# Kernel optimization log

Measured on AMD Instinct MI355X. Metric: run time of the kernel, lower is better.

The kernel has to match this reference:

```python
import math
import jax, jax.numpy as jnp
import numpy as np

N = 8192
IN_DIM = 512
INTER = 512
HID = 1024
OUT = 512
GROUPS = 16
EPS = 1e-5


def setup_inputs() -> dict:
    key = jax.random.key(0)
    ks = jax.random.split(key, 12)
    w = lambda k, shape: jax.random.normal(k, shape, jnp.float32) * 0.02
    return {
        "h": jax.random.normal(ks[0], (N, IN_DIM), jnp.float32),
        "D": jax.random.uniform(ks[1], (N, N), dtype=jnp.float32),
        "h_prime": jax.random.normal(ks[2], (N, OUT), jnp.float32),
        "Wq": w(ks[3], (INTER, IN_DIM)), "bq": jnp.zeros((INTER,), jnp.float32),
        "Wk": w(ks[4], (INTER, IN_DIM)), "bk": jnp.zeros((INTER,), jnp.float32),
        "Wv": w(ks[5], (INTER, IN_DIM)), "bv": jnp.zeros((INTER,), jnp.float32),
        "Wr": w(ks[6], (HID, INTER)), "br": jnp.zeros((HID,), jnp.float32),
        "Wc": w(ks[7], (HID, OUT)), "bc": jnp.zeros((HID,), jnp.float32),
        "Wp": w(ks[8], (OUT, 2 * HID)), "bp": jnp.zeros((OUT,), jnp.float32),
        "alpha": jnp.full((OUT,), 0.25, jnp.float32),       # PReLU per-channel slope
        "gamma": jnp.ones((OUT,), jnp.float32),             # GroupNorm weight
        "beta": jnp.zeros((OUT,), jnp.float32),             # GroupNorm bias
    }


def reference(h, D, h_prime, Wq, bq, Wk, bk, Wv, bv, Wr, br, Wc, bc, Wp, bp, alpha, gamma, beta):
    Q = h @ Wq.T + bq                                    # [N, inter]
    K = h @ Wk.T + bk
    V = h @ Wv.T + bv
    scores = (Q @ K.T) / math.sqrt(INTER)                # [N, N]
    attn = jax.nn.softmax(D * scores, axis=-1)           # decay-masked softmax
    h_ret = attn @ V                                     # [N, inter]
    h_ret = jax.nn.gelu(h_ret @ Wr.T + br, approximate=False)  # torch GELU (erf)
    h_cat = h_prime @ Wc.T + bc                          # [N, hid]
    x = jnp.concatenate([h_ret, h_cat], axis=-1) @ Wp.T + bp   # [N, out]
    x = jnp.where(x >= 0, x, alpha * x)                  # PReLU, per-channel
    # GroupNorm over [1, out, N]: stats per group over (channels_in_group, N)
    xT = x.T                                             # [out, N]
    grp = xT.reshape(GROUPS, (OUT // GROUPS) * N)
    mean = grp.mean(axis=1, keepdims=True)
    var = grp.var(axis=1, keepdims=True)
    grp = (grp - mean) * jax.lax.rsqrt(var + EPS)
    xT = grp.reshape(OUT, N) * gamma[:, None] + beta[:, None]
    return xT.T                                          # [N, out]
```

## Files before the change

kernel.cpp:

```cpp
#include <hip/hip_runtime.h>
#include <stdint.h>
#include <math.h>

typedef float f32x4 __attribute__((ext_vector_type(4)));
typedef __bf16 bf16x8 __attribute__((ext_vector_type(8)));
typedef unsigned int u32x4 __attribute__((ext_vector_type(4)));
typedef unsigned short u16;

#define DEVINL static __device__ __forceinline__

DEVINL u16 f2bf(float f) {
  union { float f; unsigned u; } x; x.f = f;
  unsigned r = x.u + 0x7fffu + ((x.u >> 16) & 1u);
  return (u16)(r >> 16);
}

DEVINL void gload_lds16(const void* g, void* l) {
  __builtin_amdgcn_global_load_lds(
      (__attribute__((address_space(1))) void*)(g),
      (__attribute__((address_space(3))) void*)(l), 16, 0, 0);
}

__global__ void cast_kernel(const float* __restrict__ src, u16* __restrict__ dst, int n) {
  int i = (blockIdx.x * 256 + threadIdx.x) * 4;
  if (i >= n) return;
  float4 v = *(const float4*)(src + i);
  u16 o[4] = { f2bf(v.x), f2bf(v.y), f2bf(v.z), f2bf(v.w) };
  *(uint64_t*)(dst + i) = *(uint64_t*)o;
}

template<int EPI>
__global__ __launch_bounds__(256, 2) void gemm_nt(
    const u16* __restrict__ A, int lda, const u16* __restrict__ B, int ldb,
    void* __restrict__ C, int ldc, int coff,
    const float* __restrict__ bias, const float* __restrict__ alpha,
    int N128, int K, float scale, int map,
    const float* __restrict__ Dmat, float* __restrict__ psum)
{
  __shared__ __align__(16) u16 at[2][128 * 64];
  __shared__ __align__(16) u16 bt[2][128 * 64];
  const int tid = threadIdx.x;
  const int w = tid >> 6, lane = tid & 63, r = lane & 15, kg = lane >> 4;
  int bm, bn;
  if (map == 1)      { const int x = blockIdx.x & 7, i = blockIdx.x >> 3; bm = x * 8 + (i >> 2); bn = i & 3; }
  else if (map == 2) { const int x = blockIdx.x & 7, i = blockIdx.x >> 3; bm = x * 8 + (i >> 6); bn = i & 63; }
  else               { bm = blockIdx.x / N128; bn = blockIdx.x % N128; }
  const int m0 = bm * 128, n0 = bn * 128;

  f32x4 acc[4][4];
  #pragma unroll
  for (int m = 0; m < 4; ++m)
    #pragma unroll
    for (int n = 0; n < 4; ++n) acc[m][n] = f32x4{0.f, 0.f, 0.f, 0.f};

  const int srow = tid >> 3, sc = tid & 7;
  const int nk = K >> 6;

  #pragma unroll
  for (int i = 0; i < 4; ++i) {
    int row = srow + i * 32, cs = (sc ^ row) & 7;
    gload_lds16(A + (size_t)(m0 + row) * lda + cs * 8, at[0] + i * 2048 + w * 512);
    gload_lds16(B + (size_t)(n0 + row) * ldb + cs * 8, bt[0] + i * 2048 + w * 512);
  }
  __syncthreads();

  for (int kt = 0; kt < nk; ++kt) {
    const int cur = kt & 1;
    if (kt + 1 < nk) {
      #pragma unroll
      for (int i = 0; i < 4; ++i) {
        int row = srow + i * 32, cs = (sc ^ row) & 7;
        int kcol = (kt + 1) * 64 + cs * 8;
        gload_lds16(A + (size_t)(m0 + row) * lda + kcol, at[cur ^ 1] + i * 2048 + w * 512);
        gload_lds16(B + (size_t)(n0 + row) * ldb + kcol, bt[cur ^ 1] + i * 2048 + w * 512);
      }
    }
    #pragma unroll
    for (int ks = 0; ks < 2; ++ks) {
      bf16x8 af[4], bff[4];
      #pragma unroll
      for (int m = 0; m < 4; ++m) {
        int row = (w >> 1) * 64 + m * 16 + r;
        int cs = ((ks * 4 + kg) ^ row) & 7;
        af[m] = *(const bf16x8*)(at[cur] + row * 64 + cs * 8);
      }
      #pragma unroll
      for (int n = 0; n < 4; ++n) {
        int row = (w & 1) * 64 + n * 16 + r;
        int cs = ((ks * 4 + kg) ^ row) & 7;
        bff[n] = *(const bf16x8*)(bt[cur] + row * 64 + cs * 8);
      }
      #pragma unroll
      for (int m = 0; m < 4; ++m)
        #pragma unroll
        for (int n = 0; n < 4; ++n)
          acc[m][n] = __builtin_amdgcn_mfma_f32_16x16x32_bf16(af[m], bff[n], acc[m][n], 0, 0, 0);
    }
    __syncthreads();
  }

  if (EPI == 6) {
    #pragma unroll
    for (int m = 0; m < 4; ++m) {
      float rs[4] = {0.f, 0.f, 0.f, 0.f};
      #pragma unroll
      for (int n = 0; n < 4; ++n) {
        const int gcol = n0 + (w & 1) * 64 + n * 16 + r;
        #pragma unroll
        for (int reg = 0; reg < 4; ++reg) {
          const int grow = m0 + (w >> 1) * 64 + m * 16 + kg * 4 + reg;
          const float dv = __builtin_nontemporal_load(Dmat + (size_t)grow * 8192 + gcol);
          const float p = __expf(acc[m][n][reg] * dv);
          rs[reg] += p;
          ((u16*)C)[(size_t)grow * ldc + gcol] = f2bf(p);
        }
      }
      #pragma unroll
      for (int reg = 0; reg < 4; ++reg) {
        float v = rs[reg];
        v += __shfl_xor(v, 1); v += __shfl_xor(v, 2);
        v += __shfl_xor(v, 4); v += __shfl_xor(v, 8);
        if (r == 0) {
          const int grow = m0 + (w >> 1) * 64 + m * 16 + kg * 4 + reg;
          psum[(size_t)grow * 128 + bn * 2 + (w & 1)] = v;
        }
      }
    }
    return;
  }

  #pragma unroll
  for (int m = 0; m < 4; ++m) {
    #pragma unroll
    for (int n = 0; n < 4; ++n) {
      const int gcol = n0 + (w & 1) * 64 + n * 16 + r;
      #pragma unroll
      for (int reg = 0; reg < 4; ++reg) {
        const int grow = m0 + (w >> 1) * 64 + m * 16 + kg * 4 + reg;
        float v = acc[m][n][reg];
        if (EPI == 0) v = (v + bias[gcol]) * scale;
        if (EPI == 1) v = v + bias[grow];
        if (EPI == 2) { v += bias[gcol]; v = 0.5f * v * (1.f + erff(v * 0.70710678118654752f)); }
        if (EPI == 5) v = v / bias[grow];
        if (EPI == 3) {
          v += bias[gcol];
          float a = alpha[gcol];
          v = (v >= 0.f) ? v : a * v;
          ((float*)C)[(size_t)grow * ldc + coff + gcol] = v;
        } else {
          ((u16*)C)[(size_t)grow * ldc + coff + gcol] = f2bf(v);
        }
      }
    }
  }
}

__global__ __launch_bounds__(256) void rowsum_kernel(const float* __restrict__ psum,
                                                     float* __restrict__ ls) {
  const int row = blockIdx.x * 4 + (threadIdx.x >> 6);
  const int lane = threadIdx.x & 63;
  const float2 v = *(const float2*)(psum + (size_t)row * 128 + lane * 2);
  float s = v.x + v.y;
  #pragma unroll
  for (int m = 1; m < 64; m <<= 1) s += __shfl_xor(s, m);
  if (lane == 0) ls[row] = s;
}

__global__ void gn_stats_kernel(const float* __restrict__ x, float* __restrict__ part) {
  const int g = blockIdx.x >> 4, ch = blockIdx.x & 15;
  const int t = threadIdx.x;
  float s = 0.f, ss = 0.f;
  const int cl = (t & 7) * 4;
  const int r0 = ch * 512 + (t >> 3);
  for (int i = 0; i < 16; ++i) {
    const float4 v = *(const float4*)(x + (size_t)(r0 + i * 32) * 512 + g * 32 + cl);
    s += v.x + v.y + v.z + v.w;
    ss += v.x * v.x + v.y * v.y + v.z * v.z + v.w * v.w;
  }
  #pragma unroll
  for (int m = 1; m < 64; m <<= 1) { s += __shfl_xor(s, m); ss += __shfl_xor(ss, m); }
  __shared__ float red[8];
  const int w = t >> 6, lane = t & 63;
  if (lane == 0) { red[w * 2] = s; red[w * 2 + 1] = ss; }
  __syncthreads();
  if (t == 0) {
    part[blockIdx.x * 2]     = red[0] + red[2] + red[4] + red[6];
    part[blockIdx.x * 2 + 1] = red[1] + red[3] + red[5] + red[7];
  }
}

__global__ void gn_finalize_kernel(const float* __restrict__ part, float* __restrict__ mv) {
  const int g = threadIdx.x;
  if (g < 16) {
    float s = 0.f, ss = 0.f;
    for (int ch = 0; ch < 16; ++ch) {
      s  += part[(g * 16 + ch) * 2];
      ss += part[(g * 16 + ch) * 2 + 1];
    }
    const float mean = s * (1.f / 262144.f);
    const float var = ss * (1.f / 262144.f) - mean * mean;
    mv[g * 2] = mean;
    mv[g * 2 + 1] = rsqrtf(var + 1e-5f);
  }
}

__global__ void gn_norm_kernel(const float* __restrict__ x, const float* __restrict__ mv,
                               const float* __restrict__ gamma, const float* __restrict__ beta,
                               float* __restrict__ out) {
  const int idx = (blockIdx.x * 256 + threadIdx.x) * 4;
  const int c = idx & 511, g = c >> 5;
  const float mean = mv[g * 2], rs = mv[g * 2 + 1];
  float4 v = *(const float4*)(x + idx);
  const float4 gm = *(const float4*)(gamma + c);
  const float4 bt = *(const float4*)(beta + c);
  v.x = (v.x - mean) * rs * gm.x + bt.x;
  v.y = (v.y - mean) * rs * gm.y + bt.y;
  v.z = (v.z - mean) * rs * gm.z + bt.z;
  v.w = (v.w - mean) * rs * gm.w + bt.w;
  *(float4*)(out + idx) = v;
}

extern "C" void kernel_launch(void* const* d_in, const int* in_sizes, int n_in,
                              void* d_out, int out_size, void* d_ws, size_t ws_size,
                              hipStream_t stream) {
  (void)in_sizes; (void)n_in; (void)out_size; (void)ws_size;
  const float* h     = (const float*)d_in[0];
  const float* Dm    = (const float*)d_in[1];
  const float* hp    = (const float*)d_in[2];
  const float* Wq    = (const float*)d_in[3];
  const float* bq    = (const float*)d_in[4];
  const float* Wk    = (const float*)d_in[5];
  const float* bk    = (const float*)d_in[6];
  const float* Wv    = (const float*)d_in[7];
  const float* bv    = (const float*)d_in[8];
  const float* Wr    = (const float*)d_in[9];
  const float* br    = (const float*)d_in[10];
  const float* Wc    = (const float*)d_in[11];
  const float* bc    = (const float*)d_in[12];
  const float* Wp    = (const float*)d_in[13];
  const float* bp    = (const float*)d_in[14];
  const float* alpha = (const float*)d_in[15];
  const float* gamma = (const float*)d_in[16];
  const float* beta  = (const float*)d_in[17];

  char* ws = (char*)d_ws;
  const size_t MB = 1ull << 20;
  u16*   P    = (u16*)(ws);
  u16*   hb   = (u16*)(ws);
  u16*   xcat = (u16*)(ws);
  float* xf   = (float*)(ws + 32 * MB);
  u16*   hpb  = (u16*)(ws + 128 * MB);
  u16*   Qb   = (u16*)(ws + 144 * MB);
  u16*   hrb  = (u16*)(ws + 144 * MB);
  u16*   Kb   = (u16*)(ws + 152 * MB);
  u16*   VTb  = (u16*)(ws + 160 * MB);
  u16*   Wqb  = (u16*)(ws + 168 * MB);
  u16*   Wkb  = Wqb + 262144;
  u16*   Wvb  = Wkb + 262144;
  u16*   Wrb  = Wvb + 262144;
  u16*   Wcb  = Wrb + 524288;
  u16*   Wpb  = Wcb + 524288;
  float* lsum = (float*)(ws + 168 * MB + 5767168);
  float* gp   = lsum + 8192;
  float* mv   = gp + 512;
  float* psum = (float*)(ws + 176 * MB);

  cast_kernel<<<4096, 256, 0, stream>>>(h, hb, 4194304);
  cast_kernel<<<4096, 256, 0, stream>>>(hp, hpb, 4194304);
  cast_kernel<<<256, 256, 0, stream>>>(Wq, Wqb, 262144);
  cast_kernel<<<256, 256, 0, stream>>>(Wk, Wkb, 262144);
  cast_kernel<<<256, 256, 0, stream>>>(Wv, Wvb, 262144);
  cast_kernel<<<512, 256, 0, stream>>>(Wr, Wrb, 524288);
  cast_kernel<<<512, 256, 0, stream>>>(Wc, Wcb, 524288);
  cast_kernel<<<1024, 256, 0, stream>>>(Wp, Wpb, 1048576);

  gemm_nt<0><<<256, 256, 0, stream>>>(hb, 512, Wqb, 512, Qb, 512, 0, bq, nullptr, 4, 512, 0.044194173824159216f, 0, nullptr, nullptr);
  gemm_nt<0><<<256, 256, 0, stream>>>(hb, 512, Wkb, 512, Kb, 512, 0, bk, nullptr, 4, 512, 1.0f, 0, nullptr, nullptr);
  gemm_nt<1><<<256, 256, 0, stream>>>(Wvb, 512, hb, 512, VTb, 8192, 0, bv, nullptr, 64, 512, 1.0f, 0, nullptr, nullptr);

  gemm_nt<6><<<4096, 256, 0, stream>>>(Qb, 512, Kb, 512, P, 8192, 0, nullptr, nullptr, 64, 512, 1.0f, 2, Dm, psum);
  rowsum_kernel<<<2048, 256, 0, stream>>>(psum, lsum);

  gemm_nt<5><<<256, 256, 0, stream>>>(P, 8192, VTb, 8192, hrb, 512, 0, lsum, nullptr, 4, 8192, 1.0f, 1, nullptr, nullptr);

  gemm_nt<2><<<512, 256, 0, stream>>>(hrb, 512, Wrb, 512, xcat, 2048, 0, br, nullptr, 8, 512, 1.0f, 0, nullptr, nullptr);
  gemm_nt<0><<<512, 256, 0, stream>>>(hpb, 512, Wcb, 512, xcat, 2048, 1024, bc, nullptr, 8, 512, 1.0f, 0, nullptr, nullptr);

  gemm_nt<3><<<256, 256, 0, stream>>>(xcat, 2048, Wpb, 2048, xf, 512, 0, bp, alpha, 4, 2048, 1.0f, 0, nullptr, nullptr);

  gn_stats_kernel<<<256, 256, 0, stream>>>(xf, gp);
  gn_finalize_kernel<<<1, 64, 0, stream>>>(gp, mv);
  gn_norm_kernel<<<4096, 256, 0, stream>>>(xf, mv, gamma, beta, (float*)d_out);
}
```

Measured before the change: 439.3 us.

## Prefetch decay matrix into registers during QK^T mainloop in dedicated kernel

Splits the score GEMM into a dedicated sgemm_exp kernel. It issues nontemporal loads of the D tile into 64 registers, spread across the K-loop iterations, so the 256MB D read overlaps with MFMA work instead of stalling in the epilogue. It also changes the block-to-XCD mapping to a 16x32 tile region per XCD pair, for better L2 reuse of Q/K. The 64 extra registers per thread may lower occupancy or cause spills under launch_bounds(256,2).

```diff
diff --git a/kernel.cpp b/kernel.cpp
--- a/kernel.cpp
+++ b/kernel.cpp
@@ -34,17 +34,15 @@
     const u16* __restrict__ A, int lda, const u16* __restrict__ B, int ldb,
     void* __restrict__ C, int ldc, int coff,
     const float* __restrict__ bias, const float* __restrict__ alpha,
-    int N128, int K, float scale, int map,
-    const float* __restrict__ Dmat, float* __restrict__ psum)
+    int N128, int K, float scale, int map)
 {
   __shared__ __align__(16) u16 at[2][128 * 64];
   __shared__ __align__(16) u16 bt[2][128 * 64];
   const int tid = threadIdx.x;
   const int w = tid >> 6, lane = tid & 63, r = lane & 15, kg = lane >> 4;
   int bm, bn;
-  if (map == 1)      { const int x = blockIdx.x & 7, i = blockIdx.x >> 3; bm = x * 8 + (i >> 2); bn = i & 3; }
-  else if (map == 2) { const int x = blockIdx.x & 7, i = blockIdx.x >> 3; bm = x * 8 + (i >> 6); bn = i & 63; }
-  else               { bm = blockIdx.x / N128; bn = blockIdx.x % N128; }
+  if (map == 1) { const int x = blockIdx.x & 7, i = blockIdx.x >> 3; bm = x * 8 + (i >> 2); bn = i & 3; }
+  else          { bm = blockIdx.x / N128; bn = blockIdx.x % N128; }
   const int m0 = bm * 128, n0 = bn * 128;
 
   f32x4 acc[4][4];
@@ -97,36 +95,6 @@
           acc[m][n] = __builtin_amdgcn_mfma_f32_16x16x32_bf16(af[m], bff[n], acc[m][n], 0, 0, 0);
     }
     __syncthreads();
-  }
-
-  if (EPI == 6) {
-    #pragma unroll
-    for (int m = 0; m < 4; ++m) {
-      float rs[4] = {0.f, 0.f, 0.f, 0.f};
-      #pragma unroll
-      for (int n = 0; n < 4; ++n) {
-        const int gcol = n0 + (w & 1) * 64 + n * 16 + r;
-        #pragma unroll
-        for (int reg = 0; reg < 4; ++reg) {
-          const int grow = m0 + (w >> 1) * 64 + m * 16 + kg * 4 + reg;
-          const float dv = __builtin_nontemporal_load(Dmat + (size_t)grow * 8192 + gcol);
-          const float p = __expf(acc[m][n][reg] * dv);
-          rs[reg] += p;
-          ((u16*)C)[(size_t)grow * ldc + gcol] = f2bf(p);
-        }
-      }
-      #pragma unroll
-      for (int reg = 0; reg < 4; ++reg) {
-        float v = rs[reg];
-        v += __shfl_xor(v, 1); v += __shfl_xor(v, 2);
-        v += __shfl_xor(v, 4); v += __shfl_xor(v, 8);
-        if (r == 0) {
-          const int grow = m0 + (w >> 1) * 64 + m * 16 + kg * 4 + reg;
-          psum[(size_t)grow * 128 + bn * 2 + (w & 1)] = v;
-        }
-      }
-    }
-    return;
   }
 
   #pragma unroll
@@ -151,6 +119,106 @@
           ((u16*)C)[(size_t)grow * ldc + coff + gcol] = f2bf(v);
         }
       }
+    }
+  }
+}
+
+__global__ __launch_bounds__(256, 2) void sgemm_exp(
+    const u16* __restrict__ A, const u16* __restrict__ B,
+    u16* __restrict__ P, const float* __restrict__ Dmat, float* __restrict__ psum)
+{
+  __shared__ __align__(16) u16 at[2][128 * 64];
+  __shared__ __align__(16) u16 bt[2][128 * 64];
+  const int tid = threadIdx.x;
+  const int w = tid >> 6, lane = tid & 63, r = lane & 15, kg = lane >> 4;
+  const int xcd = blockIdx.x & 7, i = blockIdx.x >> 3;
+  const int bm = (xcd >> 1) * 16 + (i & 15);
+  const int bn = (xcd & 1) * 32 + (i >> 4);
+  const int m0 = bm * 128, n0 = bn * 128;
+
+  f32x4 acc[4][4];
+  #pragma unroll
+  for (int m = 0; m < 4; ++m)
+    #pragma unroll
+    for (int n = 0; n < 4; ++n) acc[m][n] = f32x4{0.f, 0.f, 0.f, 0.f};
+  float dreg[64];
+
+  const int srow = tid >> 3, sc = tid & 7;
+  const int gcolb = n0 + (w & 1) * 64 + r;
+  const int growb = m0 + (w >> 1) * 64 + kg * 4;
+
+  #pragma unroll
+  for (int ii = 0; ii < 4; ++ii) {
+    int row = srow + ii * 32, cs = (sc ^ row) & 7;
+    gload_lds16(A + (size_t)(m0 + row) * 512 + cs * 8, at[0] + ii * 2048 + w * 512);
+    gload_lds16(B + (size_t)(n0 + row) * 512 + cs * 8, bt[0] + ii * 2048 + w * 512);
+  }
+  __syncthreads();
+
+  #pragma unroll
+  for (int kt = 0; kt < 8; ++kt) {
+    const int cur = kt & 1;
+    if (kt < 7) {
+      #pragma unroll
+      for (int ii = 0; ii < 4; ++ii) {
+        int row = srow + ii * 32, cs = (sc ^ row) & 7;
+        int kcol = (kt + 1) * 64 + cs * 8;
+        gload_lds16(A + (size_t)(m0 + row) * 512 + kcol, at[cur ^ 1] + ii * 2048 + w * 512);
+        gload_lds16(B + (size_t)(n0 + row) * 512 + kcol, bt[cur ^ 1] + ii * 2048 + w * 512);
+      }
+    }
+    #pragma unroll
+    for (int q = 0; q < 8; ++q) {
+      const int id = kt * 8 + q;
+      const int m = id >> 4, n = (id >> 2) & 3, reg = id & 3;
+      dreg[id] = __builtin_nontemporal_load(
+          Dmat + (size_t)(growb + m * 16 + reg) * 8192 + (gcolb + n * 16));
+    }
+    #pragma unroll
+    for (int ks = 0; ks < 2; ++ks) {
+      bf16x8 af[4], bff[4];
+      #pragma unroll
+      for (int m = 0; m < 4; ++m) {
+        int row = (w >> 1) * 64 + m * 16 + r;
+        int cs = ((ks * 4 + kg) ^ row) & 7;
+        af[m] = *(const bf16x8*)(at[cur] + row * 64 + cs * 8);
+      }
+      #pragma unroll
+      for (int n = 0; n < 4; ++n) {
+        int row = (w & 1) * 64 + n * 16 + r;
+        int cs = ((ks * 4 + kg) ^ row) & 7;
+        bff[n] = *(const bf16x8*)(bt[cur] + row * 64 + cs * 8);
+      }
+      #pragma unroll
+      for (int m = 0; m < 4; ++m)
+        #pragma unroll
+        for (int n = 0; n < 4; ++n)
+          acc[m][n] = __builtin_amdgcn_mfma_f32_16x16x32_bf16(af[m], bff[n], acc[m][n], 0, 0, 0);
+    }
+    __syncthreads();
+  }
+
+  #pragma unroll
+  for (int m = 0; m < 4; ++m) {
+    float rs[4] = {0.f, 0.f, 0.f, 0.f};
+    #pragma unroll
+    for (int n = 0; n < 4; ++n) {
+      const int gcol = gcolb + n * 16;
+      #pragma unroll
+      for (int reg = 0; reg < 4; ++reg) {
+        const int grow = growb + m * 16 + reg;
+        const float p = __expf(acc[m][n][reg] * dreg[m * 16 + n * 4 + reg]);
+        rs[reg] += p;
+        P[(size_t)grow * 8192 + gcol] = f2bf(p);
+      }
+    }
+    #pragma unroll
+    for (int reg = 0; reg < 4; ++reg) {
+      float v = rs[reg];
+      v += __shfl_xor(v, 1); v += __shfl_xor(v, 2);
+      v += __shfl_xor(v, 4); v += __shfl_xor(v, 8);
+      if (r == 0)
+        psum[(size_t)(growb + m * 16 + reg) * 128 + bn * 2 + (w & 1)] = v;
     }
   }
 }
@@ -274,19 +342,19 @@
   cast_kernel<<<512, 256, 0, stream>>>(Wc, Wcb, 524288);
   cast_kernel<<<1024, 256, 0, stream>>>(Wp, Wpb, 1048576);
 
-  gemm_nt<0><<<256, 256, 0, stream>>>(hb, 512, Wqb, 512, Qb, 512, 0, bq, nullptr, 4, 512, 0.044194173824159216f, 0, nullptr, nullptr);
-  gemm_nt<0><<<256, 256, 0, stream>>>(hb, 512, Wkb, 512, Kb, 512, 0, bk, nullptr, 4, 512, 1.0f, 0, nullptr, nullptr);
-  gemm_nt<1><<<256, 256, 0, stream>>>(Wvb, 512, hb, 512, VTb, 8192, 0, bv, nullptr, 64, 512, 1.0f, 0, nullptr, nullptr);
-
-  gemm_nt<6><<<4096, 256, 0, stream>>>(Qb, 512, Kb, 512, P, 8192, 0, nullptr, nullptr, 64, 512, 1.0f, 2, Dm, psum);
+  gemm_nt<0><<<256, 256, 0, stream>>>(hb, 512, Wqb, 512, Qb, 512, 0, bq, nullptr, 4, 512, 0.044194173824159216f, 0);
+  gemm_nt<0><<<256, 256, 0, stream>>>(hb, 512, Wkb, 512, Kb, 512, 0, bk, nullptr, 4, 512, 1.0f, 0);
+  gemm_nt<1><<<256, 256, 0, stream>>>(Wvb, 512, hb, 512, VTb, 8192, 0, bv, nullptr, 64, 512, 1.0f, 0);
+
+  sgemm_exp<<<4096, 256, 0, stream>>>(Qb, Kb, P, Dm, psum);
   rowsum_kernel<<<2048, 256, 0, stream>>>(psum, lsum);
 
-  gemm_nt<5><<<256, 256, 0, stream>>>(P, 8192, VTb, 8192, hrb, 512, 0, lsum, nullptr, 4, 8192, 1.0f, 1, nullptr, nullptr);
-
-  gemm_nt<2><<<512, 256, 0, stream>>>(hrb, 512, Wrb, 512, xcat, 2048, 0, br, nullptr, 8, 512, 1.0f, 0, nullptr, nullptr);
-  gemm_nt<0><<<512, 256, 0, stream>>>(hpb, 512, Wcb, 512, xcat, 2048, 1024, bc, nullptr, 8, 512, 1.0f, 0, nullptr, nullptr);
-
-  gemm_nt<3><<<256, 256, 0, stream>>>(xcat, 2048, Wpb, 2048, xf, 512, 0, bp, alpha, 4, 2048, 1.0f, 0, nullptr, nullptr);
+  gemm_nt<5><<<256, 256, 0, stream>>>(P, 8192, VTb, 8192, hrb, 512, 0, lsum, nullptr, 4, 8192, 1.0f, 1);
+
+  gemm_nt<2><<<512, 256, 0, stream>>>(hrb, 512, Wrb, 512, xcat, 2048, 0, br, nullptr, 8, 512, 1.0f, 0);
+  gemm_nt<0><<<512, 256, 0, stream>>>(hpb, 512, Wcb, 512, xcat, 2048, 1024, bc, nullptr, 8, 512, 1.0f, 0);
+
+  gemm_nt<3><<<256, 256, 0, stream>>>(xcat, 2048, Wpb, 2048, xf, 512, 0, bp, alpha, 4, 2048, 1.0f, 0);
 
   gn_stats_kernel<<<256, 256, 0, stream>>>(xf, gp);
   gn_finalize_kernel<<<1, 64, 0, stream>>>(gp, mv);
```

Result: slower. 455.7 us (+3.7%).
